# Kernel tuning notes

Measured on AMD Instinct MI355X. Metric: run time of the kernel, lower is better.

Reference implementation:

```python
import jax, jax.numpy as jnp
import numpy as np


def setup_inputs() -> dict:
    key = jax.random.key(0)
    k1, k2, k3, k4 = jax.random.split(key, 4)
    B, C, W, H = 4, 64, 512, 512
    cF = jax.random.normal(k1, (B, C, W, H), dtype=jnp.float32)
    sF = jax.random.uniform(k2, (B, C, W, H), dtype=jnp.float32)
    alpha = jnp.array([0.6], dtype=jnp.float32)
    # style eigenvalues: strictly > 1e-5 so k_s == C (full rank), matching the
    # module's k_s = sum(s_e > 1e-5) slicing when the style SVD is well-conditioned
    s_e = jax.random.uniform(k3, (B, C), dtype=jnp.float32) + 0.5
    s_v = jax.random.normal(k4, (B, C, C), dtype=jnp.float32)
    return {"cF": cF, "sF": sF, "alpha": alpha, "s_e": s_e, "s_v": s_v}


def reference(cF, sF, alpha, s_e, s_v):
    B, C, W, H = cF.shape
    N = W * H
    cf = cF.reshape(B, C, N)            # [B, C, WH]
    sf = sF.reshape(B, C, -1)           # [B, C, W1H1]

    # ---- whiten content ----
    c_mean = jnp.mean(cf, axis=2, keepdims=True)
    cfc = cf - c_mean                   # centered content
    # covariance + I  (I shift => all eigenvalues >= 1, so k_c == C)
    cov = jnp.einsum('bcn,bdn->bcd', cfc, cfc) / (N - 1) + jnp.eye(C, dtype=cf.dtype)
    _, c_e, c_vh = jnp.linalg.svd(cov, full_matrices=False)
    c_d = c_e ** -0.5
    # original: step2 = (Vh @ diag(c_d)) @ Vh^T  -> fuse diag as column scale
    step2 = jnp.einsum('bij,bj,blj->bil', c_vh, c_d, c_vh)
    whiten_cF = jnp.einsum('bcd,bdn->bcn', step2, cfc)

    # ---- color with style stats ----
    s_mean = jnp.mean(sf, axis=2, keepdims=True)
    s_d = s_e ** 0.5                    # k_s == C by construction of s_e
    colorM = jnp.einsum('bij,bj,blj->bil', s_v, s_d, s_v)
    target = jnp.einsum('bcd,bdn->bcn', colorM, whiten_cF) + s_mean

    a = alpha.reshape(())
    csF = a * target + (1.0 - a) * cf
    return csF.reshape(B, C, W, H).astype(jnp.float32)
```

## Files before the change

kernel.cpp:

```cpp
#include <hip/hip_runtime.h>
#include <math.h>

#define WS_G 0
#define WS_SC 16384
#define WS_SS 16640
#define WS_T 16896
#define WS_BIAS 33280
#define WS_ZERO_COUNT 16896

typedef __attribute__((ext_vector_type(8))) short bf16x8;
typedef __attribute__((ext_vector_type(16))) float f32x16;

__device__ __forceinline__ float waveRed(float v) {
#pragma unroll
    for (int o = 32; o > 0; o >>= 1) v += __shfl_down(v, o, 64);
    return v;
}

__global__ void zero_kernel(float* __restrict__ ws, int n) {
    int i = blockIdx.x * 256 + threadIdx.x;
    if (i < n) ws[i] = 0.f;
}

__global__ __launch_bounds__(256) void sum_kernel(const float* __restrict__ x,
                                                  float* __restrict__ sums, int N) {
    const int ch = blockIdx.x >> 3;
    const int part = blockIdx.x & 7;
    const int seg = N >> 3;
    const float4* p = reinterpret_cast<const float4*>(x + (size_t)ch * N + (size_t)part * seg);
    const int nf4 = seg >> 2;
    float acc = 0.f;
    for (int i = threadIdx.x; i < nf4; i += 256) {
        float4 v = p[i];
        acc += (v.x + v.y) + (v.z + v.w);
    }
    acc = waveRed(acc);
    __shared__ float red[4];
    if ((threadIdx.x & 63) == 0) red[threadIdx.x >> 6] = acc;
    __syncthreads();
    if (threadIdx.x == 0) atomicAdd(&sums[ch], (red[0] + red[1]) + (red[2] + red[3]));
}

#define GR_SLAB 1040
#define GR_PLANE 16640
__global__ __launch_bounds__(256) void gram_kernel(const float* __restrict__ cF,
                                                   float* __restrict__ G,
                                                   float* __restrict__ Sc, int N) {
    __shared__ __align__(16) char smem[2 * GR_PLANE];
    const int b = blockIdx.x >> 7;
    const int part = blockIdx.x & 127;
    const float* base = cF + (size_t)b * 64 * N + (size_t)part * (N >> 7);
    const int t = threadIdx.x;
    const int wid = t >> 6;
    const int lane = t & 63;
    const int I = (wid >> 1) << 5;
    const int Jt = (wid & 1) << 5;
    const bool diag = (I == Jt);
    const int rA = I + (lane & 31);
    const int rB = Jt + (lane & 31);
    const int sl = lane >> 5;

    f32x16 acc = {};
    float rs[8];
#pragma unroll
    for (int i = 0; i < 8; ++i) rs[i] = 0.f;

    float4 v[8];
#pragma unroll
    for (int i = 0; i < 8; ++i) {
        int f = t + 256 * i;
        v[i] = *reinterpret_cast<const float4*>(base + (size_t)(f >> 5) * N + (f & 31) * 4);
    }

    for (int c = 0; c < 16; ++c) {
        uint2 hw[8], lw[8];
#pragma unroll
        for (int i = 0; i < 8; ++i) {
            float4 x = v[i];
            rs[i] += (x.x + x.y) + (x.z + x.w);
            unsigned bx = __float_as_uint(x.x), by = __float_as_uint(x.y);
            unsigned bz = __float_as_uint(x.z), bw = __float_as_uint(x.w);
            float lx = x.x - __uint_as_float(bx & 0xffff0000u);
            float ly = x.y - __uint_as_float(by & 0xffff0000u);
            float lz = x.z - __uint_as_float(bz & 0xffff0000u);
            float lwv = x.w - __uint_as_float(bw & 0xffff0000u);
            hw[i] = make_uint2((bx >> 16) | (by & 0xffff0000u),
                               (bz >> 16) | (bw & 0xffff0000u));
            lw[i] = make_uint2((__float_as_uint(lx) >> 16) | (__float_as_uint(ly) & 0xffff0000u),
                               (__float_as_uint(lz) >> 16) | (__float_as_uint(lwv) & 0xffff0000u));
        }
        __syncthreads();
#pragma unroll
        for (int i = 0; i < 8; ++i) {
            int f = t + 256 * i;
            int row = f >> 5, col4 = f & 31;
            char* dst = smem + (col4 >> 1) * GR_SLAB + row * 16 + ((col4 & 1) << 3);
            *reinterpret_cast<uint2*>(dst) = hw[i];
            *reinterpret_cast<uint2*>(dst + GR_PLANE) = lw[i];
        }
        if (c < 15) {
            const float* gn = base + (c + 1) * 128;
#pragma unroll
            for (int i = 0; i < 8; ++i) {
                int f = t + 256 * i;
                v[i] = *reinterpret_cast<const float4*>(gn + (size_t)(f >> 5) * N + (f & 31) * 4);
            }
        }
        __syncthreads();
#pragma unroll
        for (int kc = 0; kc < 8; ++kc) {
            const char* sb = smem + (2 * kc + sl) * GR_SLAB;
            bf16x8 ahi = *reinterpret_cast<const bf16x8*>(sb + rA * 16);
            bf16x8 alo = *reinterpret_cast<const bf16x8*>(sb + GR_PLANE + rA * 16);
            bf16x8 bhi, blo;
            if (diag) {
                bhi = ahi; blo = alo;
            } else {
                bhi = *reinterpret_cast<const bf16x8*>(sb + rB * 16);
                blo = *reinterpret_cast<const bf16x8*>(sb + GR_PLANE + rB * 16);
            }
            acc = __builtin_amdgcn_mfma_f32_32x32x16_bf16(ahi, bhi, acc, 0, 0, 0);
            acc = __builtin_amdgcn_mfma_f32_32x32x16_bf16(ahi, blo, acc, 0, 0, 0);
            acc = __builtin_amdgcn_mfma_f32_32x32x16_bf16(alo, bhi, acc, 0, 0, 0);
        }
        __syncthreads();
    }

    float* Gb = G + b * 4096;
#pragma unroll
    for (int r = 0; r < 16; ++r) {
        int m = (r & 3) + 8 * (r >> 2) + 4 * (lane >> 5);
        int n = lane & 31;
        atomicAdd(&Gb[(I + m) * 64 + (Jt + n)], acc[r]);
    }
    const int baseRow = t >> 5;
#pragma unroll
    for (int i = 0; i < 8; ++i) {
        float s = rs[i];
#pragma unroll
        for (int o = 16; o > 0; o >>= 1) s += __shfl_xor(s, o);
        if ((lane & 31) == 0) atomicAdd(&Sc[b * 64 + baseRow + 8 * i], s);
    }
}

#define SSTR 68

__device__ __forceinline__ void matmul44(float* __restrict__ D, const float* __restrict__ A,
                                         const float* __restrict__ Bm, int i0, int j0) {
    float acc[4][4];
#pragma unroll
    for (int i = 0; i < 4; ++i)
#pragma unroll
        for (int j = 0; j < 4; ++j) acc[i][j] = 0.f;
    for (int k = 0; k < 64; ++k) {
        float4 bv = *reinterpret_cast<const float4*>(&Bm[k * SSTR + j0]);
        float a0 = A[(i0 + 0) * SSTR + k];
        float a1 = A[(i0 + 1) * SSTR + k];
        float a2 = A[(i0 + 2) * SSTR + k];
        float a3 = A[(i0 + 3) * SSTR + k];
        acc[0][0] += a0 * bv.x; acc[0][1] += a0 * bv.y; acc[0][2] += a0 * bv.z; acc[0][3] += a0 * bv.w;
        acc[1][0] += a1 * bv.x; acc[1][1] += a1 * bv.y; acc[1][2] += a1 * bv.z; acc[1][3] += a1 * bv.w;
        acc[2][0] += a2 * bv.x; acc[2][1] += a2 * bv.y; acc[2][2] += a2 * bv.z; acc[2][3] += a2 * bv.w;
        acc[3][0] += a3 * bv.x; acc[3][1] += a3 * bv.y; acc[3][2] += a3 * bv.z; acc[3][3] += a3 * bv.w;
    }
#pragma unroll
    for (int i = 0; i < 4; ++i)
#pragma unroll
        for (int j = 0; j < 4; ++j) D[(i0 + i) * SSTR + j0 + j] = acc[i][j];
}

__global__ __launch_bounds__(256) void solve_kernel(const float* __restrict__ G,
                                                    const float* __restrict__ Sc,
                                                    const float* __restrict__ Ss,
                                                    const float* __restrict__ alphap,
                                                    const float* __restrict__ s_e,
                                                    const float* __restrict__ s_v,
                                                    float* __restrict__ Tg,
                                                    float* __restrict__ biasg, int N) {
    __shared__ __align__(16) float Abuf[64 * SSTR];
    __shared__ __align__(16) float Ybuf[64 * SSTR];
    __shared__ __align__(16) float Tbuf[64 * SSTR];
    __shared__ __align__(16) float Wb[64 * 20];
    __shared__ float sdv[64], mcv[64], msv[64];
    __shared__ float redv;
    const int b = blockIdx.x, t = threadIdx.x;
    const int i0 = (t >> 4) << 2, j0 = (t & 15) << 2;
    const float invN = 1.f / (float)N;
    const float invNm1 = 1.f / (float)(N - 1);
    if (t < 64) {
        mcv[t] = Sc[b * 64 + t] * invN;
        msv[t] = Ss[b * 64 + t] * invN;
        sdv[t] = sqrtf(s_e[b * 64 + t]);
    }
    __syncthreads();
#pragma unroll
    for (int i = 0; i < 4; ++i) {
        float mi = mcv[i0 + i];
#pragma unroll
        for (int j = 0; j < 4; ++j) {
            float g = G[b * 4096 + (i0 + i) * 64 + j0 + j];
            float cov = (g - mi * mcv[j0 + j] * (float)N) * invNm1 + (((i0 + i) == (j0 + j)) ? 1.f : 0.f);
            Abuf[(i0 + i) * SSTR + j0 + j] = cov;
        }
    }
    __syncthreads();
    if (t < 64) {
        float d = waveRed(Abuf[t * SSTR + t]);
        if (t == 0) redv = d * (1.f / 64.f);
    }
    __syncthreads();
    const float s = redv;
    const float inv_s = 1.f / s;
#pragma unroll
    for (int i = 0; i < 4; ++i)
#pragma unroll
        for (int j = 0; j < 4; ++j) {
            Abuf[(i0 + i) * SSTR + j0 + j] *= inv_s;
            Ybuf[(i0 + i) * SSTR + j0 + j] = ((i0 + i) == (j0 + j)) ? 1.f : 0.f;
        }
    __syncthreads();
    const int kr = t >> 2;
    const int cw = (t & 3) << 2;
    for (int it = 0; it < 3; ++it) {
        matmul44(Tbuf, Ybuf, Ybuf, i0, j0);
        __syncthreads();
        for (int lb = 0; lb < 4; ++lb) {
            const int cb = lb << 4;
            float w0 = 0.f, w1 = 0.f, w2 = 0.f, w3 = 0.f;
            for (int j = 0; j < 64; ++j) {
                float a = Abuf[kr * SSTR + j];
                float4 tv = *reinterpret_cast<const float4*>(&Tbuf[j * SSTR + cb + cw]);
                w0 += a * tv.x; w1 += a * tv.y; w2 += a * tv.z; w3 += a * tv.w;
            }
            Wb[kr * 20 + cw + 0] = ((kr == cb + cw + 0) ? 1.5f : 0.f) - 0.5f * w0;
            Wb[kr * 20 + cw + 1] = ((kr == cb + cw + 1) ? 1.5f : 0.f) - 0.5f * w1;
            Wb[kr * 20 + cw + 2] = ((kr == cb + cw + 2) ? 1.5f : 0.f) - 0.5f * w2;
            Wb[kr * 20 + cw + 3] = ((kr == cb + cw + 3) ? 1.5f : 0.f) - 0.5f * w3;
            __syncthreads();
            float y0 = 0.f, y1 = 0.f, y2 = 0.f, y3 = 0.f;
            for (int k = 0; k < 64; ++k) {
                float a = Ybuf[kr * SSTR + k];
                float4 wv = *reinterpret_cast<const float4*>(&Wb[k * 20 + cw]);
                y0 += a * wv.x; y1 += a * wv.y; y2 += a * wv.z; y3 += a * wv.w;
            }
            Tbuf[kr * SSTR + cb + cw + 0] = y0;
            Tbuf[kr * SSTR + cb + cw + 1] = y1;
            Tbuf[kr * SSTR + cb + cw + 2] = y2;
            Tbuf[kr * SSTR + cb + cw + 3] = y3;
            __syncthreads();
        }
#pragma unroll
        for (int i = 0; i < 4; ++i)
#pragma unroll
            for (int j = 0; j < 4; ++j)
                Ybuf[(i0 + i) * SSTR + j0 + j] = Tbuf[(i0 + i) * SSTR + j0 + j];
        __syncthreads();
    }
    for (int i = 0; i < 16; ++i) {
        int idx = t + 256 * i;
        Abuf[(idx >> 6) * SSTR + (idx & 63)] = s_v[b * 4096 + idx];
    }
    __syncthreads();
    {
        float acc[4][4];
#pragma unroll
        for (int i = 0; i < 4; ++i)
#pragma unroll
            for (int j = 0; j < 4; ++j) acc[i][j] = 0.f;
        for (int k = 0; k < 64; ++k) {
            float sd = sdv[k];
            float a0 = Abuf[(i0 + 0) * SSTR + k] * sd;
            float a1 = Abuf[(i0 + 1) * SSTR + k] * sd;
            float a2 = Abuf[(i0 + 2) * SSTR + k] * sd;
            float a3 = Abuf[(i0 + 3) * SSTR + k] * sd;
            float c0v = Abuf[(j0 + 0) * SSTR + k];
            float c1v = Abuf[(j0 + 1) * SSTR + k];
            float c2v = Abuf[(j0 + 2) * SSTR + k];
            float c3v = Abuf[(j0 + 3) * SSTR + k];
            acc[0][0] += a0 * c0v; acc[0][1] += a0 * c1v; acc[0][2] += a0 * c2v; acc[0][3] += a0 * c3v;
            acc[1][0] += a1 * c0v; acc[1][1] += a1 * c1v; acc[1][2] += a1 * c2v; acc[1][3] += a1 * c3v;
            acc[2][0] += a2 * c0v; acc[2][1] += a2 * c1v; acc[2][2] += a2 * c2v; acc[2][3] += a2 * c3v;
            acc[3][0] += a3 * c0v; acc[3][1] += a3 * c1v; acc[3][2] += a3 * c2v; acc[3][3] += a3 * c3v;
        }
        __syncthreads();
#pragma unroll
        for (int i = 0; i < 4; ++i)
#pragma unroll
            for (int j = 0; j < 4; ++j) Tbuf[(i0 + i) * SSTR + j0 + j] = acc[i][j];
    }
    __syncthreads();
    matmul44(Abuf, Tbuf, Ybuf, i0, j0);
    __syncthreads();
    const float alpha_v = alphap[0];
    const float fac = alpha_v / sqrtf(s);
#pragma unroll
    for (int i = 0; i < 4; ++i)
#pragma unroll
        for (int j = 0; j < 4; ++j) {
            float m = Abuf[(i0 + i) * SSTR + j0 + j] * fac;
            if ((i0 + i) == (j0 + j)) m += 1.f - alpha_v;
            Tg[b * 4096 + (i0 + i) * 64 + j0 + j] = m;
        }
    if (t < 64) {
        float acc = 0.f;
        for (int d = 0; d < 64; ++d) acc += Abuf[t * SSTR + d] * mcv[d];
        biasg[b * 64 + t] = alpha_v * msv[t] - fac * acc;
    }
}

#define ASTR 132
__global__ __launch_bounds__(256) void apply_kernel(const float* __restrict__ cF,
                                                    const float* __restrict__ T,
                                                    const float* __restrict__ bias,
                                                    float* __restrict__ out, int N) {
    __shared__ __align__(16) float tile[64 * ASTR];
    __shared__ float Tl[64 * 65];
    __shared__ float bl[64];
    const int b = blockIdx.x >> 9;
    const int part = blockIdx.x & 511;
    const int chunk = N >> 9;
    const float* src = cF + (size_t)b * 64 * N + (size_t)part * chunk;
    float* dst = out + (size_t)b * 64 * N + (size_t)part * chunk;
    const int t = threadIdx.x;
    for (int i = 0; i < 16; ++i) {
        int idx = t + 256 * i;
        Tl[(idx >> 6) * 65 + (idx & 63)] = T[b * 4096 + idx];
    }
    if (t < 64) bl[t] = bias[b * 64 + t];
    const int x0 = (t & 7) * 4;
    const int cA = (t >> 3) * 2;
    for (int sub = 0; sub < 4; ++sub) {
        __syncthreads();
        const float* gsrc = src + sub * 128;
#pragma unroll
        for (int i = 0; i < 8; ++i) {
            int f = t + 256 * i;
            int row = f >> 5, col4 = f & 31;
            *reinterpret_cast<float4*>(&tile[row * ASTR + col4 * 4]) =
                *reinterpret_cast<const float4*>(gsrc + (size_t)row * N + col4 * 4);
        }
        __syncthreads();
        float b0 = bl[cA], b1 = bl[cA + 1];
        float4 acc0[4], acc1[4];
#pragma unroll
        for (int g = 0; g < 4; ++g) {
            acc0[g] = make_float4(b0, b0, b0, b0);
            acc1[g] = make_float4(b1, b1, b1, b1);
        }
        const float* t0 = &Tl[cA * 65];
        const float* t1 = &Tl[(cA + 1) * 65];
#pragma unroll 2
        for (int k = 0; k < 64; ++k) {
            float a0 = t0[k], a1 = t1[k];
            const float* trow = &tile[k * ASTR + x0];
#pragma unroll
            for (int g = 0; g < 4; ++g) {
                float4 v = *reinterpret_cast<const float4*>(trow + 32 * g);
                acc0[g].x += a0 * v.x; acc0[g].y += a0 * v.y; acc0[g].z += a0 * v.z; acc0[g].w += a0 * v.w;
                acc1[g].x += a1 * v.x; acc1[g].y += a1 * v.y; acc1[g].z += a1 * v.z; acc1[g].w += a1 * v.w;
            }
        }
        float* d0 = dst + (size_t)cA * N + sub * 128 + x0;
        float* d1 = dst + (size_t)(cA + 1) * N + sub * 128 + x0;
#pragma unroll
        for (int g = 0; g < 4; ++g) {
            *reinterpret_cast<float4*>(d0 + 32 * g) = acc0[g];
            *reinterpret_cast<float4*>(d1 + 32 * g) = acc1[g];
        }
    }
}

extern "C" void kernel_launch(void* const* d_in, const int* in_sizes, int n_in,
                              void* d_out, int out_size, void* d_ws, size_t ws_size,
                              hipStream_t stream) {
    const float* cF = (const float*)d_in[0];
    const float* sF = (const float*)d_in[1];
    const float* alpha = (const float*)d_in[2];
    const float* s_e = (const float*)d_in[3];
    const float* s_v = (const float*)d_in[4];
    float* out = (float*)d_out;
    float* ws = (float*)d_ws;
    const int B = 4, C = 64;
    const int N = in_sizes[0] / (B * C);
    float* G = ws + WS_G;
    float* Sc = ws + WS_SC;
    float* Ss = ws + WS_SS;
    float* T = ws + WS_T;
    float* bias = ws + WS_BIAS;
    hipLaunchKernelGGL(zero_kernel, dim3(66), dim3(256), 0, stream, ws, WS_ZERO_COUNT);
    hipLaunchKernelGGL(sum_kernel, dim3(B * C * 8), dim3(256), 0, stream, sF, Ss, N);
    hipLaunchKernelGGL(gram_kernel, dim3(B * 128), dim3(256), 0, stream, cF, G, Sc, N);
    hipLaunchKernelGGL(solve_kernel, dim3(B), dim3(256), 0, stream, G, Sc, Ss, alpha, s_e, s_v, T, bias, N);
    hipLaunchKernelGGL(apply_kernel, dim3(B * 512), dim3(256), 0, stream, cF, T, bias, out, N);
}
```

Baseline: 757.3 us.

## Merge style-sum into gram kernel and move apply GEMM to split-bf16 MFMA

The separate sF mean-reduction kernel is folded into the gram kernel as extra blocks of one launch, so the style sum and the content gram can run at the same time. The apply kernel is rewritten to split T and the content tile into bf16 hi/lo pairs and compute the 64x64 transform with three MFMA 32x32x16 ops per k-step, replacing scalar FP32 FMAs. It uses smaller per-block tiles (128 pixels) and more blocks. The trade-off is bf16x3 accuracy instead of full FP32, and output stores are now scalar and strided rather than float4.

Result: faster. 737.2 us (-2.7%).

```diff
diff --git a/kernel.cpp b/kernel.cpp
--- a/kernel.cpp
+++ b/kernel.cpp
@@ -22,35 +22,37 @@
     if (i < n) ws[i] = 0.f;
 }
 
-__global__ __launch_bounds__(256) void sum_kernel(const float* __restrict__ x,
-                                                  float* __restrict__ sums, int N) {
-    const int ch = blockIdx.x >> 3;
-    const int part = blockIdx.x & 7;
-    const int seg = N >> 3;
-    const float4* p = reinterpret_cast<const float4*>(x + (size_t)ch * N + (size_t)part * seg);
-    const int nf4 = seg >> 2;
-    float acc = 0.f;
-    for (int i = threadIdx.x; i < nf4; i += 256) {
-        float4 v = p[i];
-        acc += (v.x + v.y) + (v.z + v.w);
-    }
-    acc = waveRed(acc);
-    __shared__ float red[4];
-    if ((threadIdx.x & 63) == 0) red[threadIdx.x >> 6] = acc;
-    __syncthreads();
-    if (threadIdx.x == 0) atomicAdd(&sums[ch], (red[0] + red[1]) + (red[2] + red[3]));
-}
-
 #define GR_SLAB 1040
 #define GR_PLANE 16640
-__global__ __launch_bounds__(256) void gram_kernel(const float* __restrict__ cF,
-                                                   float* __restrict__ G,
-                                                   float* __restrict__ Sc, int N) {
+__global__ __launch_bounds__(256) void pre_kernel(const float* __restrict__ cF,
+                                                  const float* __restrict__ sF,
+                                                  float* __restrict__ G,
+                                                  float* __restrict__ Sc,
+                                                  float* __restrict__ Ss, int N) {
     __shared__ __align__(16) char smem[2 * GR_PLANE];
-    const int b = blockIdx.x >> 7;
-    const int part = blockIdx.x & 127;
+    const int t = threadIdx.x;
+    if (blockIdx.x < 2048) {
+        const int ch = blockIdx.x >> 3;
+        const int part = blockIdx.x & 7;
+        const int seg = N >> 3;
+        const float4* p = reinterpret_cast<const float4*>(sF + (size_t)ch * N + (size_t)part * seg);
+        const int nf4 = seg >> 2;
+        float acc = 0.f;
+        for (int i = t; i < nf4; i += 256) {
+            float4 v = p[i];
+            acc += (v.x + v.y) + (v.z + v.w);
+        }
+        acc = waveRed(acc);
+        float* red = reinterpret_cast<float*>(smem);
+        if ((t & 63) == 0) red[t >> 6] = acc;
+        __syncthreads();
+        if (t == 0) atomicAdd(&Ss[ch], (red[0] + red[1]) + (red[2] + red[3]));
+        return;
+    }
+    const int bid2 = blockIdx.x - 2048;
+    const int b = bid2 >> 7;
+    const int part = bid2 & 127;
     const float* base = cF + (size_t)b * 64 * N + (size_t)part * (N >> 7);
-    const int t = threadIdx.x;
     const int wid = t >> 6;
     const int lane = t & 63;
     const int I = (wid >> 1) << 5;
@@ -308,65 +310,92 @@
     }
 }
 
-#define ASTR 132
+#define APX 128
+#define XSTR 72
 __global__ __launch_bounds__(256) void apply_kernel(const float* __restrict__ cF,
-                                                    const float* __restrict__ T,
-                                                    const float* __restrict__ bias,
+                                                    const float* __restrict__ Tg,
+                                                    const float* __restrict__ biasg,
                                                     float* __restrict__ out, int N) {
-    __shared__ __align__(16) float tile[64 * ASTR];
-    __shared__ float Tl[64 * 65];
+    __shared__ __align__(16) unsigned short sx[2][APX][XSTR];
     __shared__ float bl[64];
-    const int b = blockIdx.x >> 9;
-    const int part = blockIdx.x & 511;
-    const int chunk = N >> 9;
-    const float* src = cF + (size_t)b * 64 * N + (size_t)part * chunk;
-    float* dst = out + (size_t)b * 64 * N + (size_t)part * chunk;
+    const int b = blockIdx.x >> 11;
+    const int part = blockIdx.x & 2047;
+    const float* src = cF + (size_t)b * 64 * N + (size_t)part * APX;
+    float* dst = out + (size_t)b * 64 * N + (size_t)part * APX;
     const int t = threadIdx.x;
-    for (int i = 0; i < 16; ++i) {
-        int idx = t + 256 * i;
-        Tl[(idx >> 6) * 65 + (idx & 63)] = T[b * 4096 + idx];
-    }
-    if (t < 64) bl[t] = bias[b * 64 + t];
-    const int x0 = (t & 7) * 4;
-    const int cA = (t >> 3) * 2;
-    for (int sub = 0; sub < 4; ++sub) {
-        __syncthreads();
-        const float* gsrc = src + sub * 128;
-#pragma unroll
-        for (int i = 0; i < 8; ++i) {
-            int f = t + 256 * i;
-            int row = f >> 5, col4 = f & 31;
-            *reinterpret_cast<float4*>(&tile[row * ASTR + col4 * 4]) =
-                *reinterpret_cast<const float4*>(gsrc + (size_t)row * N + col4 * 4);
-        }
-        __syncthreads();
-        float b0 = bl[cA], b1 = bl[cA + 1];
-        float4 acc0[4], acc1[4];
-#pragma unroll
-        for (int g = 0; g < 4; ++g) {
-            acc0[g] = make_float4(b0, b0, b0, b0);
-            acc1[g] = make_float4(b1, b1, b1, b1);
-        }
-        const float* t0 = &Tl[cA * 65];
-        const float* t1 = &Tl[(cA + 1) * 65];
-#pragma unroll 2
-        for (int k = 0; k < 64; ++k) {
-            float a0 = t0[k], a1 = t1[k];
-            const float* trow = &tile[k * ASTR + x0];
-#pragma unroll
-            for (int g = 0; g < 4; ++g) {
-                float4 v = *reinterpret_cast<const float4*>(trow + 32 * g);
-                acc0[g].x += a0 * v.x; acc0[g].y += a0 * v.y; acc0[g].z += a0 * v.z; acc0[g].w += a0 * v.w;
-                acc1[g].x += a1 * v.x; acc1[g].y += a1 * v.y; acc1[g].z += a1 * v.z; acc1[g].w += a1 * v.w;
+    const int lane = t & 63;
+    const int wid = t >> 6;
+    if (t < 64) bl[t] = biasg[b * 64 + t];
+
+    const int I = (wid & 1) << 5;
+    const int xb0 = (wid >> 1) << 6;
+    const int kb = (lane >> 5) << 3;
+    bf16x8 th[4], tl[4];
+    {
+        const float* Trow = Tg + b * 4096 + (size_t)(I + (lane & 31)) * 64;
+#pragma unroll
+        for (int ks = 0; ks < 4; ++ks) {
+            float4 u0 = *reinterpret_cast<const float4*>(Trow + ks * 16 + kb);
+            float4 u1 = *reinterpret_cast<const float4*>(Trow + ks * 16 + kb + 4);
+            float v[8] = {u0.x, u0.y, u0.z, u0.w, u1.x, u1.y, u1.z, u1.w};
+#pragma unroll
+            for (int j = 0; j < 8; ++j) {
+                unsigned u = __float_as_uint(v[j]);
+                th[ks][j] = (short)(u >> 16);
+                float r = v[j] - __uint_as_float(u & 0xffff0000u);
+                tl[ks][j] = (short)(__float_as_uint(r) >> 16);
             }
         }
-        float* d0 = dst + (size_t)cA * N + sub * 128 + x0;
-        float* d1 = dst + (size_t)(cA + 1) * N + sub * 128 + x0;
-#pragma unroll
-        for (int g = 0; g < 4; ++g) {
-            *reinterpret_cast<float4*>(d0 + 32 * g) = acc0[g];
-            *reinterpret_cast<float4*>(d1 + 32 * g) = acc1[g];
-        }
+    }
+
+#pragma unroll
+    for (int i = 0; i < 4; ++i) {
+        int u = t + 256 * i;
+        int kp = u >> 5;
+        int x0 = (u & 31) << 2;
+        const float* ra = src + (size_t)(2 * kp) * N + x0;
+        float4 va = *reinterpret_cast<const float4*>(ra);
+        float4 vb = *reinterpret_cast<const float4*>(ra + N);
+        float av[4] = {va.x, va.y, va.z, va.w};
+        float bv[4] = {vb.x, vb.y, vb.z, vb.w};
+#pragma unroll
+        for (int j = 0; j < 4; ++j) {
+            unsigned ua = __float_as_uint(av[j]);
+            unsigned ub = __float_as_uint(bv[j]);
+            float ral = av[j] - __uint_as_float(ua & 0xffff0000u);
+            float rbl = bv[j] - __uint_as_float(ub & 0xffff0000u);
+            unsigned hi = (ua >> 16) | (ub & 0xffff0000u);
+            unsigned lo = (__float_as_uint(ral) >> 16) | (__float_as_uint(rbl) & 0xffff0000u);
+            *reinterpret_cast<unsigned*>(&sx[0][x0 + j][2 * kp]) = hi;
+            *reinterpret_cast<unsigned*>(&sx[1][x0 + j][2 * kp]) = lo;
+        }
+    }
+    __syncthreads();
+
+    f32x16 acc0 = {}, acc1 = {};
+    const int xA = xb0 + (lane & 31);
+#pragma unroll
+    for (int ks = 0; ks < 4; ++ks) {
+        const int ko = ks * 16 + kb;
+        bf16x8 bh0 = *reinterpret_cast<const bf16x8*>(&sx[0][xA][ko]);
+        bf16x8 bL0 = *reinterpret_cast<const bf16x8*>(&sx[1][xA][ko]);
+        bf16x8 bh1 = *reinterpret_cast<const bf16x8*>(&sx[0][xA + 32][ko]);
+        bf16x8 bL1 = *reinterpret_cast<const bf16x8*>(&sx[1][xA + 32][ko]);
+        acc0 = __builtin_amdgcn_mfma_f32_32x32x16_bf16(th[ks], bh0, acc0, 0, 0, 0);
+        acc0 = __builtin_amdgcn_mfma_f32_32x32x16_bf16(th[ks], bL0, acc0, 0, 0, 0);
+        acc0 = __builtin_amdgcn_mfma_f32_32x32x16_bf16(tl[ks], bh0, acc0, 0, 0, 0);
+        acc1 = __builtin_amdgcn_mfma_f32_32x32x16_bf16(th[ks], bh1, acc1, 0, 0, 0);
+        acc1 = __builtin_amdgcn_mfma_f32_32x32x16_bf16(th[ks], bL1, acc1, 0, 0, 0);
+        acc1 = __builtin_amdgcn_mfma_f32_32x32x16_bf16(tl[ks], bh1, acc1, 0, 0, 0);
+    }
+
+#pragma unroll
+    for (int r = 0; r < 16; ++r) {
+        int m = (r & 3) + 8 * (r >> 2) + 4 * (lane >> 5);
+        float bb = bl[I + m];
+        float* dr = dst + (size_t)(I + m) * N;
+        dr[xA] = acc0[r] + bb;
+        dr[xA + 32] = acc1[r] + bb;
     }
 }
 
@@ -388,8 +417,7 @@
     float* T = ws + WS_T;
     float* bias = ws + WS_BIAS;
     hipLaunchKernelGGL(zero_kernel, dim3(66), dim3(256), 0, stream, ws, WS_ZERO_COUNT);
-    hipLaunchKernelGGL(sum_kernel, dim3(B * C * 8), dim3(256), 0, stream, sF, Ss, N);
-    hipLaunchKernelGGL(gram_kernel, dim3(B * 128), dim3(256), 0, stream, cF, G, Sc, N);
+    hipLaunchKernelGGL(pre_kernel, dim3(2048 + B * 128), dim3(256), 0, stream, cF, sF, G, Sc, Ss, N);
     hipLaunchKernelGGL(solve_kernel, dim3(B), dim3(256), 0, stream, G, Sc, Ss, alpha, s_e, s_v, T, bias, N);
-    hipLaunchKernelGGL(apply_kernel, dim3(B * 512), dim3(256), 0, stream, cF, T, bias, out, N);
-}
+    hipLaunchKernelGGL(apply_kernel, dim3(B * 2048), dim3(256), 0, stream, cF, T, bias, out, N);
+}
```
